# Kernel tuning notes

Hardware: AMD Instinct MI355X
Metric: run time of the kernel (lower is better)

The kernel has to match this reference:

```python
import jax, jax.numpy as jnp
import numpy as np

EPS = 1e-09
NUM_ITERS = 3

def squash_axis2(s):
    # Faithful to CapsuleLayer.squash: reduces over dim=2 of the (5-D) torch
    # tensor; here s is [B, 1, J, V] and dim=2 is the num_units axis J.
    mag_sq = jnp.sum(s * s, axis=2, keepdims=True)
    mag = jnp.sqrt(mag_sq + EPS)
    return mag_sq / (1.0 + mag_sq) * (s / mag)

def setup_inputs() -> dict:
    key = jax.random.key(0)
    k1, k2 = jax.random.split(key)
    B, I, J, D, V = 64, 2048, 32, 128, 32
    x = jax.random.normal(k1, (B, I, D), dtype=jnp.float32)
    # W stored as [I, J, D, V] (torch param is [1, I, J, unit_size, vec_len])
    W = jax.random.normal(k2, (I, J, D, V), dtype=jnp.float32)
    return {"x": x, "W": W}

def reference(x, W):
    B, I, D = x.shape
    J, V = W.shape[1], W.shape[3]
    # u_hat[b,i,j,v] = sum_d W[i,j,d,v] * x[b,i,d]  (torch: W^T @ x per capsule)
    u_hat = jnp.einsum('ijdv,bid->bijv', W, x)  # [B, I, J, V]
    u_hat_sg = jax.lax.stop_gradient(u_hat)
    b_ij = jnp.zeros((B, I, J), dtype=x.dtype)
    v_j = None
    for it in range(NUM_ITERS):
        c_ij = jax.nn.softmax(b_ij, axis=1)  # softmax over num_caps_i (dim=1)
        uh = u_hat if it == NUM_ITERS - 1 else u_hat_sg
        s_j = jnp.sum(c_ij[..., None] * uh, axis=1, keepdims=True)  # [B,1,J,V]
        v_j = squash_axis2(s_j)  # [B,1,J,V] (squash reduces over J, as in source)
        if it < NUM_ITERS - 1:
            # agreement: <u_hat_i, v_j> -> [B,I,J], mean over batch, broadcast-add
            agree = jnp.einsum('bijv,bjv->bij', u_hat_sg, v_j[:, 0])
            b_ij = b_ij + jnp.mean(agree, axis=0, keepdims=True)
    return v_j[:, 0]  # squeeze -> [B, J, V]
```

## Files before the change

### kernel.cpp

```cpp
#include <hip/hip_runtime.h>
#include <math.h>

#define NI 2048
#define NJ 32
#define ND 128
#define NV 32
#define NB 64

typedef _Float16 f16x8 __attribute__((ext_vector_type(8)));
typedef float f32x4 __attribute__((ext_vector_type(4)));

__device__ __forceinline__ unsigned short f2h(float f) {
  _Float16 h = (_Float16)f;
  return __builtin_bit_cast(unsigned short, h);
}
__device__ __forceinline__ float h2f(unsigned short u) {
  return (float)__builtin_bit_cast(_Float16, u);
}

#define LOADKS(dst, wp, ks)                                                    \
  {                                                                            \
    _Pragma("unroll") for (int n = 0; n < 2; ++n) {                            \
      const float* bp =                                                        \
          (wp) + (size_t)((ks) * 32 + lg * 8) * NV + n * 16 + li;              \
      _Pragma("unroll") for (int e = 0; e < 8; ++e)                            \
          dst[n * 8 + e] = bp[(size_t)e * NV];                                 \
    }                                                                          \
  }

__global__ __launch_bounds__(256, 2) void k_uhat(
    const float* __restrict__ x, const float* __restrict__ W,
    unsigned short* __restrict__ uhat) {
  const int i = blockIdx.x;
  const int tid = threadIdx.x;
  const int wave = tid >> 6;
  const int lane = tid & 63;
  __shared__ unsigned short xs[64][136];

  {
    const int b = tid >> 2;
    const int d0 = (tid & 3) * 32;
    const float* xp = x + ((size_t)b * NI + i) * ND + d0;
#pragma unroll
    for (int c2 = 0; c2 < 8; ++c2) {
      f32x4 v = *(const f32x4*)(xp + 4 * c2);
      ushort4 h;
      h.x = f2h(v.x); h.y = f2h(v.y); h.z = f2h(v.z); h.w = f2h(v.w);
      *(ushort4*)&xs[b][d0 + 4 * c2] = h;
    }
  }
  __syncthreads();

  const int li = lane & 15;
  const int lg = lane >> 4;

  f16x8 afrag[4][4];
#pragma unroll
  for (int m = 0; m < 4; ++m)
#pragma unroll
    for (int ks = 0; ks < 4; ++ks)
      afrag[m][ks] = *(const f16x8*)&xs[m * 16 + li][ks * 32 + lg * 8];

  const float* wp0 = W + ((size_t)i * NJ + wave * 8) * (ND * NV);
  float raw[2][16];
  LOADKS(raw[0], wp0, 0)

#pragma unroll 1
  for (int jj = 0; jj < 8; ++jj) {
    const int j = wave * 8 + jj;
    const float* wp = wp0 + (size_t)jj * (ND * NV);
    f32x4 acc[4][2];
#pragma unroll
    for (int m = 0; m < 4; ++m)
#pragma unroll
      for (int n = 0; n < 2; ++n)
        acc[m][n] = (f32x4){0.f, 0.f, 0.f, 0.f};

#pragma unroll
    for (int ks = 0; ks < 4; ++ks) {
      const int cur = ks & 1;
      const int nxt = cur ^ 1;
      if (ks < 3) {
        LOADKS(raw[nxt], wp, ks + 1)
      } else {
        const int jn = (jj + 1) & 7;
        const float* wpn = wp0 + (size_t)jn * (ND * NV);
        LOADKS(raw[nxt], wpn, 0)
      }
      f16x8 bfrag[2];
#pragma unroll
      for (int n = 0; n < 2; ++n) {
        f16x8 bf;
#pragma unroll
        for (int e = 0; e < 8; ++e) bf[e] = (_Float16)raw[cur][n * 8 + e];
        bfrag[n] = bf;
      }
#pragma unroll
      for (int m = 0; m < 4; ++m)
#pragma unroll
        for (int n = 0; n < 2; ++n)
          acc[m][n] = __builtin_amdgcn_mfma_f32_16x16x32_f16(
              afrag[m][ks], bfrag[n], acc[m][n], 0, 0, 0);
    }

    unsigned short* up = uhat + ((size_t)i * NJ + j) * (NB * NV);
#pragma unroll
    for (int m = 0; m < 4; ++m)
#pragma unroll
      for (int n = 0; n < 2; ++n) {
        const int v0 = n * 16 + li;
        const int b0 = m * 16 + lg * 4;
#pragma unroll
        for (int r = 0; r < 4; ++r)
          up[(size_t)(b0 + r) * NV + v0] = f2h(acc[m][n][r]);
      }
  }
}

__global__ __launch_bounds__(256) void k_pass0(
    const unsigned short* __restrict__ uhat, float* __restrict__ spart) {
  const int j = blockIdx.x & 31;
  const int ch = blockIdx.x >> 5;
  const int tid = threadIdx.x;
  const int f0 = tid * 8;
  float acc[8] = {0, 0, 0, 0, 0, 0, 0, 0};
  const int i0 = ch * 64;
#pragma unroll 4
  for (int ii = 0; ii < 64; ++ii) {
    const int i = i0 + ii;
    const uint4 q = *(const uint4*)(uhat + ((size_t)(i * NJ + j)) * (NB * NV) + f0);
    acc[0] += h2f((unsigned short)(q.x & 0xffff));
    acc[1] += h2f((unsigned short)(q.x >> 16));
    acc[2] += h2f((unsigned short)(q.y & 0xffff));
    acc[3] += h2f((unsigned short)(q.y >> 16));
    acc[4] += h2f((unsigned short)(q.z & 0xffff));
    acc[5] += h2f((unsigned short)(q.z >> 16));
    acc[6] += h2f((unsigned short)(q.w & 0xffff));
    acc[7] += h2f((unsigned short)(q.w >> 16));
  }
  const int b = f0 >> 5;
  const int v0 = f0 & 31;
  float* sp = spart + (size_t)ch * (NB * NJ * NV) + (size_t)b * (NJ * NV) + j * NV + v0;
  *(f32x4*)sp = (f32x4){acc[0], acc[1], acc[2], acc[3]};
  *(f32x4*)(sp + 4) = (f32x4){acc[4], acc[5], acc[6], acc[7]};
}

__global__ __launch_bounds__(256) void k_route(
    const unsigned short* __restrict__ uhat, const float* __restrict__ vprev,
    const float* __restrict__ bin, float* __restrict__ bout,
    float* __restrict__ spart, float* __restrict__ Zpart) {
  const int j = blockIdx.x & 31;
  const int ch = blockIdx.x >> 5;
  const int tid = threadIdx.x;
  const int wave = tid >> 6;
  const int lane = tid & 63;
  const int f0 = tid * 8;
  const int b = f0 >> 5;
  const int v0 = f0 & 31;
  __shared__ float red[2][4];

  const float* vp = vprev + (size_t)b * (NJ * NV) + j * NV + v0;
  const f32x4 vva = *(const f32x4*)vp;
  const f32x4 vvb = *(const f32x4*)(vp + 4);

  float acc[8] = {0, 0, 0, 0, 0, 0, 0, 0};
  float zacc = 0.0f;
  const int i0 = ch * 64;
#pragma unroll 2
  for (int ii = 0; ii < 64; ++ii) {
    const int i = i0 + ii;
    const float bprev = bin ? bin[(size_t)j * NI + i] : 0.0f;
    const uint4 q = *(const uint4*)(uhat + ((size_t)(i * NJ + j)) * (NB * NV) + f0);
    float h[8];
    h[0] = h2f((unsigned short)(q.x & 0xffff));
    h[1] = h2f((unsigned short)(q.x >> 16));
    h[2] = h2f((unsigned short)(q.y & 0xffff));
    h[3] = h2f((unsigned short)(q.y >> 16));
    h[4] = h2f((unsigned short)(q.z & 0xffff));
    h[5] = h2f((unsigned short)(q.z >> 16));
    h[6] = h2f((unsigned short)(q.w & 0xffff));
    h[7] = h2f((unsigned short)(q.w >> 16));
    float dp = h[0] * vva.x + h[1] * vva.y + h[2] * vva.z + h[3] * vva.w +
               h[4] * vvb.x + h[5] * vvb.y + h[6] * vvb.z + h[7] * vvb.w;
#pragma unroll
    for (int off = 32; off > 0; off >>= 1) dp += __shfl_xor(dp, off);
    const int par = ii & 1;
    if (lane == 0) red[par][wave] = dp;
    __syncthreads();
    const float agree = red[par][0] + red[par][1] + red[par][2] + red[par][3];
    const float bnew = bprev + agree * (1.0f / 64.0f);
    const float w = expf(bnew);
    if (tid == 0) bout[(size_t)j * NI + i] = bnew;
#pragma unroll
    for (int e = 0; e < 8; ++e) acc[e] = fmaf(w, h[e], acc[e]);
    zacc += w;
  }
  if (tid == 0) Zpart[ch * NJ + j] = zacc;
  float* sp = spart + (size_t)ch * (NB * NJ * NV) + (size_t)b * (NJ * NV) + j * NV + v0;
  *(f32x4*)sp = (f32x4){acc[0], acc[1], acc[2], acc[3]};
  *(f32x4*)(sp + 4) = (f32x4){acc[4], acc[5], acc[6], acc[7]};
}

__global__ __launch_bounds__(1024) void k_squash(
    const float* __restrict__ spart, const float* __restrict__ Zpart,
    const float scale0, float* __restrict__ vout) {
  const int b = blockIdx.x;
  const int tid = threadIdx.x;
  const int j = tid >> 5;
  const int v = tid & 31;
  __shared__ float zs[NJ];
  if (Zpart != nullptr) {
    if (tid < NJ) {
      float z = 0.0f;
#pragma unroll
      for (int ch = 0; ch < 32; ++ch) z += Zpart[ch * NJ + tid];
      zs[tid] = 1.0f / z;
    }
    __syncthreads();
  }
  const float scale = (Zpart != nullptr) ? zs[j] : scale0;
  float s = 0.0f;
#pragma unroll 8
  for (int ch = 0; ch < 32; ++ch)
    s += spart[(size_t)ch * (NB * NJ * NV) + (size_t)b * (NJ * NV) + tid];
  s *= scale;
  __shared__ float sq[NJ][NV + 1];
  sq[j][v] = s * s;
  __syncthreads();
#pragma unroll
  for (int off = 16; off > 0; off >>= 1) {
    if (j < off) sq[j][v] += sq[j + off][v];
    __syncthreads();
  }
  const float msq = sq[0][v];
  const float f = msq / ((1.0f + msq) * sqrtf(msq + 1e-9f));
  vout[(size_t)b * (NJ * NV) + tid] = f * s;
}

extern "C" void kernel_launch(void* const* d_in, const int* in_sizes, int n_in,
                              void* d_out, int out_size, void* d_ws, size_t ws_size,
                              hipStream_t stream) {
  (void)in_sizes; (void)n_in; (void)out_size; (void)ws_size;
  const float* x = (const float*)d_in[0];
  const float* W = (const float*)d_in[1];
  float* out = (float*)d_out;

  char* ws = (char*)d_ws;
  const size_t UHAT_BYTES = (size_t)NI * NJ * NB * NV * 2;
  unsigned short* uhat = (unsigned short*)ws;
  float* bbuf = (float*)(ws + UHAT_BYTES);
  float* spart = bbuf + (size_t)NI * NJ;
  float* vt = spart + (size_t)32 * NB * NJ * NV;
  float* Zpart = vt + (size_t)NB * NJ * NV;

  k_uhat<<<dim3(NI), dim3(256), 0, stream>>>(x, W, uhat);

  k_pass0<<<dim3(1024), dim3(256), 0, stream>>>(uhat, spart);
  k_squash<<<dim3(NB), dim3(1024), 0, stream>>>(spart, nullptr, 1.0f / NI, vt);

  k_route<<<dim3(1024), dim3(256), 0, stream>>>(uhat, vt, nullptr, bbuf, spart, Zpart);
  k_squash<<<dim3(NB), dim3(1024), 0, stream>>>(spart, Zpart, 0.0f, vt);

  k_route<<<dim3(1024), dim3(256), 0, stream>>>(uhat, vt, bbuf, bbuf, spart, Zpart);
  k_squash<<<dim3(NB), dim3(1024), 0, stream>>>(spart, Zpart, 0.0f, out);
}
```

Baseline: 506.8 us.

## Assign one wave per i-slice in routing kernels to drop block barriers

Routing and pass-0 kernels now give each wave its own 16-row slice of i, with each lane owning one batch element and all 32 v values. The agreement dot product then reduces entirely within a wave by shuffles, which removes the per-iteration shared-memory write and __syncthreads. The cost is four times more partial sums (128 chunks) for the squash kernel to reduce, and more registers per thread for the 32-wide accumulators. Separately, W and x loads in k_uhat become nontemporal and expf is replaced by __expf.

```diff
diff --git a/kernel.cpp b/kernel.cpp
--- a/kernel.cpp
+++ b/kernel.cpp
@@ -6,6 +6,7 @@
 #define ND 128
 #define NV 32
 #define NB 64
+#define NCW 128
 
 typedef _Float16 f16x8 __attribute__((ext_vector_type(8)));
 typedef float f32x4 __attribute__((ext_vector_type(4)));
@@ -16,6 +17,16 @@
 }
 __device__ __forceinline__ float h2f(unsigned short u) {
   return (float)__builtin_bit_cast(_Float16, u);
+}
+__device__ __forceinline__ void unpack8(uint4 q, float* h) {
+  h[0] = h2f((unsigned short)(q.x & 0xffff));
+  h[1] = h2f((unsigned short)(q.x >> 16));
+  h[2] = h2f((unsigned short)(q.y & 0xffff));
+  h[3] = h2f((unsigned short)(q.y >> 16));
+  h[4] = h2f((unsigned short)(q.z & 0xffff));
+  h[5] = h2f((unsigned short)(q.z >> 16));
+  h[6] = h2f((unsigned short)(q.w & 0xffff));
+  h[7] = h2f((unsigned short)(q.w >> 16));
 }
 
 #define LOADKS(dst, wp, ks)                                                    \
@@ -24,7 +35,7 @@
       const float* bp =                                                        \
           (wp) + (size_t)((ks) * 32 + lg * 8) * NV + n * 16 + li;              \
       _Pragma("unroll") for (int e = 0; e < 8; ++e)                            \
-          dst[n * 8 + e] = bp[(size_t)e * NV];                                 \
+          dst[n * 8 + e] = __builtin_nontemporal_load(bp + (size_t)e * NV);    \
     }                                                                          \
   }
 
@@ -43,7 +54,7 @@
     const float* xp = x + ((size_t)b * NI + i) * ND + d0;
 #pragma unroll
     for (int c2 = 0; c2 < 8; ++c2) {
-      f32x4 v = *(const f32x4*)(xp + 4 * c2);
+      f32x4 v = __builtin_nontemporal_load((const f32x4*)(xp + 4 * c2));
       ushort4 h;
       h.x = f2h(v.x); h.y = f2h(v.y); h.z = f2h(v.z); h.w = f2h(v.w);
       *(ushort4*)&xs[b][d0 + 4 * c2] = h;
@@ -121,28 +132,34 @@
     const unsigned short* __restrict__ uhat, float* __restrict__ spart) {
   const int j = blockIdx.x & 31;
   const int ch = blockIdx.x >> 5;
-  const int tid = threadIdx.x;
-  const int f0 = tid * 8;
-  float acc[8] = {0, 0, 0, 0, 0, 0, 0, 0};
-  const int i0 = ch * 64;
+  const int w = threadIdx.x >> 6;
+  const int lane = threadIdx.x & 63;
+  const int cw = ch * 4 + w;
+  const int b = lane;
+
+  float acc[32];
+#pragma unroll
+  for (int v = 0; v < 32; ++v) acc[v] = 0.f;
+  const int i0 = ch * 64 + w * 16;
+
 #pragma unroll 4
-  for (int ii = 0; ii < 64; ++ii) {
+  for (int ii = 0; ii < 16; ++ii) {
     const int i = i0 + ii;
-    const uint4 q = *(const uint4*)(uhat + ((size_t)(i * NJ + j)) * (NB * NV) + f0);
-    acc[0] += h2f((unsigned short)(q.x & 0xffff));
-    acc[1] += h2f((unsigned short)(q.x >> 16));
-    acc[2] += h2f((unsigned short)(q.y & 0xffff));
-    acc[3] += h2f((unsigned short)(q.y >> 16));
-    acc[4] += h2f((unsigned short)(q.z & 0xffff));
-    acc[5] += h2f((unsigned short)(q.z >> 16));
-    acc[6] += h2f((unsigned short)(q.w & 0xffff));
-    acc[7] += h2f((unsigned short)(q.w >> 16));
-  }
-  const int b = f0 >> 5;
-  const int v0 = f0 & 31;
-  float* sp = spart + (size_t)ch * (NB * NJ * NV) + (size_t)b * (NJ * NV) + j * NV + v0;
-  *(f32x4*)sp = (f32x4){acc[0], acc[1], acc[2], acc[3]};
-  *(f32x4*)(sp + 4) = (f32x4){acc[4], acc[5], acc[6], acc[7]};
+    const unsigned short* up = uhat + ((size_t)(i * NJ + j)) * (NB * NV) + b * NV;
+    const uint4 q0 = *(const uint4*)(up);
+    const uint4 q1 = *(const uint4*)(up + 8);
+    const uint4 q2 = *(const uint4*)(up + 16);
+    const uint4 q3 = *(const uint4*)(up + 24);
+    float h[32];
+    unpack8(q0, h); unpack8(q1, h + 8); unpack8(q2, h + 16); unpack8(q3, h + 24);
+#pragma unroll
+    for (int v = 0; v < 32; ++v) acc[v] += h[v];
+  }
+  float* sp = spart + ((size_t)cw * NB + b) * (NJ * NV) + j * NV;
+#pragma unroll
+  for (int q = 0; q < 8; ++q)
+    *(f32x4*)(sp + q * 4) =
+        (f32x4){acc[q * 4], acc[q * 4 + 1], acc[q * 4 + 2], acc[q * 4 + 3]};
 }
 
 __global__ __launch_bounds__(256) void k_route(
@@ -151,54 +168,58 @@
     float* __restrict__ spart, float* __restrict__ Zpart) {
   const int j = blockIdx.x & 31;
   const int ch = blockIdx.x >> 5;
-  const int tid = threadIdx.x;
-  const int wave = tid >> 6;
-  const int lane = tid & 63;
-  const int f0 = tid * 8;
-  const int b = f0 >> 5;
-  const int v0 = f0 & 31;
-  __shared__ float red[2][4];
-
-  const float* vp = vprev + (size_t)b * (NJ * NV) + j * NV + v0;
-  const f32x4 vva = *(const f32x4*)vp;
-  const f32x4 vvb = *(const f32x4*)(vp + 4);
-
-  float acc[8] = {0, 0, 0, 0, 0, 0, 0, 0};
-  float zacc = 0.0f;
-  const int i0 = ch * 64;
-#pragma unroll 2
-  for (int ii = 0; ii < 64; ++ii) {
+  const int w = threadIdx.x >> 6;
+  const int lane = threadIdx.x & 63;
+  const int cw = ch * 4 + w;
+  const int b = lane;
+
+  float vv[32];
+  {
+    const float* vp = vprev + ((size_t)b * NJ + j) * NV;
+#pragma unroll
+    for (int q = 0; q < 8; ++q) {
+      const f32x4 t = *(const f32x4*)(vp + q * 4);
+      vv[q * 4 + 0] = t.x; vv[q * 4 + 1] = t.y;
+      vv[q * 4 + 2] = t.z; vv[q * 4 + 3] = t.w;
+    }
+  }
+  float acc[32];
+#pragma unroll
+  for (int v = 0; v < 32; ++v) acc[v] = 0.f;
+  float zacc = 0.f;
+  const int i0 = ch * 64 + w * 16;
+  const float* binj = bin ? (bin + (size_t)j * NI) : nullptr;
+  float* boutj = bout + (size_t)j * NI;
+
+#pragma unroll 4
+  for (int ii = 0; ii < 16; ++ii) {
     const int i = i0 + ii;
-    const float bprev = bin ? bin[(size_t)j * NI + i] : 0.0f;
-    const uint4 q = *(const uint4*)(uhat + ((size_t)(i * NJ + j)) * (NB * NV) + f0);
-    float h[8];
-    h[0] = h2f((unsigned short)(q.x & 0xffff));
-    h[1] = h2f((unsigned short)(q.x >> 16));
-    h[2] = h2f((unsigned short)(q.y & 0xffff));
-    h[3] = h2f((unsigned short)(q.y >> 16));
-    h[4] = h2f((unsigned short)(q.z & 0xffff));
-    h[5] = h2f((unsigned short)(q.z >> 16));
-    h[6] = h2f((unsigned short)(q.w & 0xffff));
-    h[7] = h2f((unsigned short)(q.w >> 16));
-    float dp = h[0] * vva.x + h[1] * vva.y + h[2] * vva.z + h[3] * vva.w +
-               h[4] * vvb.x + h[5] * vvb.y + h[6] * vvb.z + h[7] * vvb.w;
+    const float bprev = binj ? binj[i] : 0.0f;
+    const unsigned short* up = uhat + ((size_t)(i * NJ + j)) * (NB * NV) + b * NV;
+    const uint4 q0 = *(const uint4*)(up);
+    const uint4 q1 = *(const uint4*)(up + 8);
+    const uint4 q2 = *(const uint4*)(up + 16);
+    const uint4 q3 = *(const uint4*)(up + 24);
+    float h[32];
+    unpack8(q0, h); unpack8(q1, h + 8); unpack8(q2, h + 16); unpack8(q3, h + 24);
+    float dp = 0.f;
+#pragma unroll
+    for (int v = 0; v < 32; ++v) dp = fmaf(h[v], vv[v], dp);
 #pragma unroll
     for (int off = 32; off > 0; off >>= 1) dp += __shfl_xor(dp, off);
-    const int par = ii & 1;
-    if (lane == 0) red[par][wave] = dp;
-    __syncthreads();
-    const float agree = red[par][0] + red[par][1] + red[par][2] + red[par][3];
-    const float bnew = bprev + agree * (1.0f / 64.0f);
-    const float w = expf(bnew);
-    if (tid == 0) bout[(size_t)j * NI + i] = bnew;
-#pragma unroll
-    for (int e = 0; e < 8; ++e) acc[e] = fmaf(w, h[e], acc[e]);
-    zacc += w;
-  }
-  if (tid == 0) Zpart[ch * NJ + j] = zacc;
-  float* sp = spart + (size_t)ch * (NB * NJ * NV) + (size_t)b * (NJ * NV) + j * NV + v0;
-  *(f32x4*)sp = (f32x4){acc[0], acc[1], acc[2], acc[3]};
-  *(f32x4*)(sp + 4) = (f32x4){acc[4], acc[5], acc[6], acc[7]};
+    const float bnew = bprev + dp * (1.0f / 64.0f);
+    const float wexp = __expf(bnew);
+    if (lane == 0) boutj[i] = bnew;
+#pragma unroll
+    for (int v = 0; v < 32; ++v) acc[v] = fmaf(wexp, h[v], acc[v]);
+    zacc += wexp;
+  }
+  if (lane == 0) Zpart[cw * NJ + j] = zacc;
+  float* sp = spart + ((size_t)cw * NB + b) * (NJ * NV) + j * NV;
+#pragma unroll
+  for (int q = 0; q < 8; ++q)
+    *(f32x4*)(sp + q * 4) =
+        (f32x4){acc[q * 4], acc[q * 4 + 1], acc[q * 4 + 2], acc[q * 4 + 3]};
 }
 
 __global__ __launch_bounds__(1024) void k_squash(
@@ -212,8 +233,8 @@
   if (Zpart != nullptr) {
     if (tid < NJ) {
       float z = 0.0f;
-#pragma unroll
-      for (int ch = 0; ch < 32; ++ch) z += Zpart[ch * NJ + tid];
+#pragma unroll 8
+      for (int ch = 0; ch < NCW; ++ch) z += Zpart[ch * NJ + tid];
       zs[tid] = 1.0f / z;
     }
     __syncthreads();
@@ -221,7 +242,7 @@
   const float scale = (Zpart != nullptr) ? zs[j] : scale0;
   float s = 0.0f;
 #pragma unroll 8
-  for (int ch = 0; ch < 32; ++ch)
+  for (int ch = 0; ch < NCW; ++ch)
     s += spart[(size_t)ch * (NB * NJ * NV) + (size_t)b * (NJ * NV) + tid];
   s *= scale;
   __shared__ float sq[NJ][NV + 1];
@@ -250,7 +271,7 @@
   unsigned short* uhat = (unsigned short*)ws;
   float* bbuf = (float*)(ws + UHAT_BYTES);
   float* spart = bbuf + (size_t)NI * NJ;
-  float* vt = spart + (size_t)32 * NB * NJ * NV;
+  float* vt = spart + (size_t)NCW * NB * NJ * NV;
   float* Zpart = vt + (size_t)NB * NJ * NV;
 
   k_uhat<<<dim3(NI), dim3(256), 0, stream>>>(x, W, uhat);
```

Measured after the change: 590.9 us. 16.6% more time.

## Batch routing dot-product reductions in groups of eight and double i-chunks

Applied to the files above, without the earlier changes.

The routing kernel now loads eight capsules' u_hat values at once, computes their partial dot products, and reduces all eight through shared memory with two barriers per group. Before, it took a block barrier for every capsule. The number of i-chunks doubles to 64 so that twice as many blocks run, and the squash kernels sum over more partials. W and x loads in the u_hat kernel now use nontemporal hints. The changes add register pressure from holding 64 unpacked floats per thread, and they enlarge the partial-sum buffers and the final reduction.

```diff
diff --git a/kernel.cpp b/kernel.cpp
--- a/kernel.cpp
+++ b/kernel.cpp
@@ -6,6 +6,7 @@
 #define ND 128
 #define NV 32
 #define NB 64
+#define NCH 64
 
 typedef _Float16 f16x8 __attribute__((ext_vector_type(8)));
 typedef float f32x4 __attribute__((ext_vector_type(4)));
@@ -16,6 +17,16 @@
 }
 __device__ __forceinline__ float h2f(unsigned short u) {
   return (float)__builtin_bit_cast(_Float16, u);
+}
+__device__ __forceinline__ void unpack8(uint4 q, float* h) {
+  h[0] = h2f((unsigned short)(q.x & 0xffff));
+  h[1] = h2f((unsigned short)(q.x >> 16));
+  h[2] = h2f((unsigned short)(q.y & 0xffff));
+  h[3] = h2f((unsigned short)(q.y >> 16));
+  h[4] = h2f((unsigned short)(q.z & 0xffff));
+  h[5] = h2f((unsigned short)(q.z >> 16));
+  h[6] = h2f((unsigned short)(q.w & 0xffff));
+  h[7] = h2f((unsigned short)(q.w >> 16));
 }
 
 #define LOADKS(dst, wp, ks)                                                    \
@@ -24,7 +35,7 @@
       const float* bp =                                                        \
           (wp) + (size_t)((ks) * 32 + lg * 8) * NV + n * 16 + li;              \
       _Pragma("unroll") for (int e = 0; e < 8; ++e)                            \
-          dst[n * 8 + e] = bp[(size_t)e * NV];                                 \
+          dst[n * 8 + e] = __builtin_nontemporal_load(bp + (size_t)e * NV);    \
     }                                                                          \
   }
 
@@ -43,7 +54,7 @@
     const float* xp = x + ((size_t)b * NI + i) * ND + d0;
 #pragma unroll
     for (int c2 = 0; c2 < 8; ++c2) {
-      f32x4 v = *(const f32x4*)(xp + 4 * c2);
+      f32x4 v = __builtin_nontemporal_load((const f32x4*)(xp + 4 * c2));
       ushort4 h;
       h.x = f2h(v.x); h.y = f2h(v.y); h.z = f2h(v.z); h.w = f2h(v.w);
       *(ushort4*)&xs[b][d0 + 4 * c2] = h;
@@ -124,19 +135,15 @@
   const int tid = threadIdx.x;
   const int f0 = tid * 8;
   float acc[8] = {0, 0, 0, 0, 0, 0, 0, 0};
-  const int i0 = ch * 64;
+  const int i0 = ch * 32;
 #pragma unroll 4
-  for (int ii = 0; ii < 64; ++ii) {
+  for (int ii = 0; ii < 32; ++ii) {
     const int i = i0 + ii;
     const uint4 q = *(const uint4*)(uhat + ((size_t)(i * NJ + j)) * (NB * NV) + f0);
-    acc[0] += h2f((unsigned short)(q.x & 0xffff));
-    acc[1] += h2f((unsigned short)(q.x >> 16));
-    acc[2] += h2f((unsigned short)(q.y & 0xffff));
-    acc[3] += h2f((unsigned short)(q.y >> 16));
-    acc[4] += h2f((unsigned short)(q.z & 0xffff));
-    acc[5] += h2f((unsigned short)(q.z >> 16));
-    acc[6] += h2f((unsigned short)(q.w & 0xffff));
-    acc[7] += h2f((unsigned short)(q.w >> 16));
+    float h[8];
+    unpack8(q, h);
+#pragma unroll
+    for (int e = 0; e < 8; ++e) acc[e] += h[e];
   }
   const int b = f0 >> 5;
   const int v0 = f0 & 31;
@@ -157,43 +164,62 @@
   const int f0 = tid * 8;
   const int b = f0 >> 5;
   const int v0 = f0 & 31;
-  __shared__ float red[2][4];
+
+  __shared__ float dp_lds[8][256];
+  __shared__ float agree_lds[8];
 
   const float* vp = vprev + (size_t)b * (NJ * NV) + j * NV + v0;
   const f32x4 vva = *(const f32x4*)vp;
   const f32x4 vvb = *(const f32x4*)(vp + 4);
 
   float acc[8] = {0, 0, 0, 0, 0, 0, 0, 0};
-  float zacc = 0.0f;
-  const int i0 = ch * 64;
-#pragma unroll 2
-  for (int ii = 0; ii < 64; ++ii) {
-    const int i = i0 + ii;
-    const float bprev = bin ? bin[(size_t)j * NI + i] : 0.0f;
-    const uint4 q = *(const uint4*)(uhat + ((size_t)(i * NJ + j)) * (NB * NV) + f0);
-    float h[8];
-    h[0] = h2f((unsigned short)(q.x & 0xffff));
-    h[1] = h2f((unsigned short)(q.x >> 16));
-    h[2] = h2f((unsigned short)(q.y & 0xffff));
-    h[3] = h2f((unsigned short)(q.y >> 16));
-    h[4] = h2f((unsigned short)(q.z & 0xffff));
-    h[5] = h2f((unsigned short)(q.z >> 16));
-    h[6] = h2f((unsigned short)(q.w & 0xffff));
-    h[7] = h2f((unsigned short)(q.w >> 16));
-    float dp = h[0] * vva.x + h[1] * vva.y + h[2] * vva.z + h[3] * vva.w +
-               h[4] * vvb.x + h[5] * vvb.y + h[6] * vvb.z + h[7] * vvb.w;
-#pragma unroll
-    for (int off = 32; off > 0; off >>= 1) dp += __shfl_xor(dp, off);
-    const int par = ii & 1;
-    if (lane == 0) red[par][wave] = dp;
-    __syncthreads();
-    const float agree = red[par][0] + red[par][1] + red[par][2] + red[par][3];
-    const float bnew = bprev + agree * (1.0f / 64.0f);
-    const float w = expf(bnew);
-    if (tid == 0) bout[(size_t)j * NI + i] = bnew;
-#pragma unroll
-    for (int e = 0; e < 8; ++e) acc[e] = fmaf(w, h[e], acc[e]);
-    zacc += w;
+  float zacc = 0.f;
+  const int i0 = ch * 32;
+  const float* binj = bin ? (bin + (size_t)j * NI) : nullptr;
+  float* boutj = bout + (size_t)j * NI;
+
+#pragma unroll 1
+  for (int g = 0; g < 4; ++g) {
+    const int ig = i0 + g * 8;
+    float hall[8][8];
+    float dp[8];
+#pragma unroll
+    for (int ii = 0; ii < 8; ++ii) {
+      const uint4 q =
+          *(const uint4*)(uhat + ((size_t)((ig + ii) * NJ + j)) * (NB * NV) + f0);
+      unpack8(q, hall[ii]);
+      float d = hall[ii][0] * vva.x + hall[ii][1] * vva.y +
+                hall[ii][2] * vva.z + hall[ii][3] * vva.w +
+                hall[ii][4] * vvb.x + hall[ii][5] * vvb.y +
+                hall[ii][6] * vvb.z + hall[ii][7] * vvb.w;
+      dp[ii] = d;
+    }
+#pragma unroll
+    for (int ii = 0; ii < 8; ++ii) dp_lds[ii][tid] = dp[ii];
+    __syncthreads();
+#pragma unroll
+    for (int r = 0; r < 2; ++r) {
+      const int ii = wave * 2 + r;
+      float s = dp_lds[ii][lane] + dp_lds[ii][lane + 64] +
+                dp_lds[ii][lane + 128] + dp_lds[ii][lane + 192];
+#pragma unroll
+      for (int off = 32; off > 0; off >>= 1) s += __shfl_xor(s, off);
+      if (lane == 0) agree_lds[ii] = s;
+    }
+    __syncthreads();
+#pragma unroll
+    for (int ii = 0; ii < 8; ++ii) {
+      const float bprev = binj ? binj[ig + ii] : 0.0f;
+      const float bnew = bprev + agree_lds[ii] * (1.0f / 64.0f);
+      const float wexp = __expf(bnew);
+      zacc += wexp;
+#pragma unroll
+      for (int e = 0; e < 8; ++e) acc[e] = fmaf(wexp, hall[ii][e], acc[e]);
+    }
+    if (tid < 8) {
+      const float bprev = binj ? binj[ig + tid] : 0.0f;
+      boutj[ig + tid] = bprev + agree_lds[tid] * (1.0f / 64.0f);
+    }
   }
   if (tid == 0) Zpart[ch * NJ + j] = zacc;
   float* sp = spart + (size_t)ch * (NB * NJ * NV) + (size_t)b * (NJ * NV) + j * NV + v0;
@@ -212,8 +238,8 @@
   if (Zpart != nullptr) {
     if (tid < NJ) {
       float z = 0.0f;
-#pragma unroll
-      for (int ch = 0; ch < 32; ++ch) z += Zpart[ch * NJ + tid];
+#pragma unroll 8
+      for (int ch = 0; ch < NCH; ++ch) z += Zpart[ch * NJ + tid];
       zs[tid] = 1.0f / z;
     }
     __syncthreads();
@@ -221,7 +247,7 @@
   const float scale = (Zpart != nullptr) ? zs[j] : scale0;
   float s = 0.0f;
 #pragma unroll 8
-  for (int ch = 0; ch < 32; ++ch)
+  for (int ch = 0; ch < NCH; ++ch)
     s += spart[(size_t)ch * (NB * NJ * NV) + (size_t)b * (NJ * NV) + tid];
   s *= scale;
   __shared__ float sq[NJ][NV + 1];
@@ -250,17 +276,17 @@
   unsigned short* uhat = (unsigned short*)ws;
   float* bbuf = (float*)(ws + UHAT_BYTES);
   float* spart = bbuf + (size_t)NI * NJ;
-  float* vt = spart + (size_t)32 * NB * NJ * NV;
+  float* vt = spart + (size_t)NCH * NB * NJ * NV;
   float* Zpart = vt + (size_t)NB * NJ * NV;
 
   k_uhat<<<dim3(NI), dim3(256), 0, stream>>>(x, W, uhat);
 
-  k_pass0<<<dim3(1024), dim3(256), 0, stream>>>(uhat, spart);
+  k_pass0<<<dim3(NCH * NJ), dim3(256), 0, stream>>>(uhat, spart);
   k_squash<<<dim3(NB), dim3(1024), 0, stream>>>(spart, nullptr, 1.0f / NI, vt);
 
-  k_route<<<dim3(1024), dim3(256), 0, stream>>>(uhat, vt, nullptr, bbuf, spart, Zpart);
+  k_route<<<dim3(NCH * NJ), dim3(256), 0, stream>>>(uhat, vt, nullptr, bbuf, spart, Zpart);
   k_squash<<<dim3(NB), dim3(1024), 0, stream>>>(spart, Zpart, 0.0f, vt);
 
-  k_route<<<dim3(1024), dim3(256), 0, stream>>>(uhat, vt, bbuf, bbuf, spart, Zpart);
+  k_route<<<dim3(NCH * NJ), dim3(256), 0, stream>>>(uhat, vt, bbuf, bbuf, spart, Zpart);
   k_squash<<<dim3(NB), dim3(1024), 0, stream>>>(spart, Zpart, 0.0f, out);
 }
```

Result: slower. 574.1 us (+13.3%).
